# Kernel optimization log

Hardware: AMD Instinct MI355X
Metric: run time of the kernel (lower is better)

The kernel has to match this reference:

```python
import jax, jax.numpy as jnp
import numpy as np

N_NODES = 50000
N_EDGES = 600000
NFEAT = 256
NHID = 128
NCLASS = 40


def setup_inputs() -> dict:
    key = jax.random.key(0)
    ks = jax.random.split(key, 10)
    x = jax.random.normal(ks[0], (N_NODES, NFEAT), dtype=jnp.float32)
    edge_src = jax.random.randint(ks[1], (N_EDGES,), 0, N_NODES, dtype=jnp.int32)
    edge_dst = jax.random.randint(ks[2], (N_EDGES,), 0, N_NODES, dtype=jnp.int32)
    # normalized adjacency weights (positive, ~1/deg scale)
    edge_weight = jax.random.uniform(ks[3], (N_EDGES,), dtype=jnp.float32) * 0.2
    # GraphConvolution params (Glorot-ish init)
    W1 = jax.random.normal(ks[4], (NFEAT, NHID), dtype=jnp.float32) / np.float32(np.sqrt(NFEAT))
    b1 = jnp.zeros((NHID,), dtype=jnp.float32)
    W2 = jax.random.normal(ks[5], (NHID, NHID), dtype=jnp.float32) / np.float32(np.sqrt(NHID))
    b2 = jnp.zeros((NHID,), dtype=jnp.float32)
    W3 = jax.random.normal(ks[6], (NHID, NCLASS), dtype=jnp.float32) / np.float32(np.sqrt(NHID))
    b3 = jnp.zeros((NCLASS,), dtype=jnp.float32)
    return {"x": x, "edge_weight": edge_weight, "W1": W1, "b1": b1,
            "W2": W2, "b2": b2, "W3": W3, "b3": b3,
            "edge_src": edge_src, "edge_dst": edge_dst}


def _gcn_layer(h, W, b, edge_src, edge_dst, edge_weight):
    # support = h @ W ; out = spmm(adj, support) + b
    support = h @ W                                   # [N, out]
    msgs = support[edge_src] * edge_weight[:, None]   # [E, out]
    agg = jax.ops.segment_sum(msgs, edge_dst, num_segments=N_NODES)
    return agg + b


def reference(x, edge_weight, W1, b1, W2, b2, W3, b3, edge_src, edge_dst):
    # eval mode: F.dropout(training=False) is identity
    h = jax.nn.relu(_gcn_layer(x, W1, b1, edge_src, edge_dst, edge_weight))
    h = jax.nn.relu(_gcn_layer(h, W2, b2, edge_src, edge_dst, edge_weight))
    h = _gcn_layer(h, W3, b3, edge_src, edge_dst, edge_weight)
    return jax.nn.log_softmax(h, axis=1)
```

## Files before the change

### kernel.cpp

```cpp
#include <hip/hip_runtime.h>
#include <hip/hip_bf16.h>
#include <math.h>

#define N_NODES 50000
#define N_EDGES 600000
#define NFEAT   256
#define NHID    128
#define NCLASS  40
#define E_PAD_MAX (N_EDGES + 7 * N_NODES)
#define GEMM_BLOCKS  ((N_NODES + 63) / 64)
#define NBUCK 196
#define EPB_A 2048
#define BUCK_CAP 4096

typedef __attribute__((ext_vector_type(8))) short bf16x8;
typedef __attribute__((ext_vector_type(4))) float f32x4;
typedef __attribute__((ext_vector_type(2))) float f32x2;

__device__ inline ushort f2bf(float f) {
    uint u = __float_as_uint(f);
    uint r = (u + 0x7fffu + ((u >> 16) & 1u)) >> 16;
    return (ushort)r;
}

__global__ __launch_bounds__(256) void scatter_binA(const int* __restrict__ src,
                                                    const int* __restrict__ dst,
                                                    const float* __restrict__ w,
                                                    int* __restrict__ bucket_cnt,
                                                    int2* __restrict__ staging, int E) {
    __shared__ int lh[NBUCK];
    int tid = threadIdx.x;
    for (int b = tid; b < NBUCK; b += 256) lh[b] = 0;
    __syncthreads();
    int base = blockIdx.x * EPB_A;
    int d[8];
    #pragma unroll
    for (int j = 0; j < 8; ++j) {
        int i = base + j * 256 + tid;
        d[j] = (i < E) ? dst[i] : -1;
        if (d[j] >= 0) atomicAdd(&lh[d[j] >> 8], 1);
    }
    __syncthreads();
    for (int b = tid; b < NBUCK; b += 256) {
        int c = lh[b];
        lh[b] = c ? (b * BUCK_CAP + atomicAdd(&bucket_cnt[b], c)) : 0;
    }
    __syncthreads();
    #pragma unroll
    for (int j = 0; j < 8; ++j) {
        int i = base + j * 256 + tid;
        if (d[j] >= 0) {
            int slot = atomicAdd(&lh[d[j] >> 8], 1);
            uint rec = ((uint)f2bf(w[i]) << 16) | (uint)src[i];
            staging[slot] = make_int2((int)rec, d[j] & 255);
        }
    }
}

__global__ __launch_bounds__(256) void bucket_hist_cvtw(const int* __restrict__ bucket_cnt,
                                                        const int2* __restrict__ staging,
                                                        int* __restrict__ bsum, int nb,
                                                        const float* __restrict__ W1,
                                                        const float* __restrict__ W2,
                                                        const float* __restrict__ W3,
                                                        ushort* __restrict__ BT1,
                                                        ushort* __restrict__ BT2,
                                                        ushort* __restrict__ BT3) {
    if ((int)blockIdx.x >= nb) {
        int idx = ((int)blockIdx.x - nb) * 256 + threadIdx.x;
        if (idx < 32768) {
            int nr = idx >> 8, k = idx & 255;
            BT1[idx] = f2bf(W1[(size_t)k * 128 + nr]);
        } else if (idx < 49152) {
            int t = idx - 32768;
            int nr = t >> 7, k = t & 127;
            BT2[t] = f2bf(W2[(size_t)k * 128 + nr]);
        } else if (idx < 57344) {
            int t = idx - 49152;
            int nr = t >> 7, k = t & 127;
            BT3[t] = (nr < 40) ? f2bf(W3[(size_t)k * 40 + nr]) : (ushort)0;
        }
        return;
    }
    __shared__ int hist[256];
    __shared__ int red[4];
    int tid = threadIdx.x;
    hist[tid] = 0;
    __syncthreads();
    int b = blockIdx.x;
    int c = bucket_cnt[b];
    const int2* st = staging + (size_t)b * BUCK_CAP;
    for (int p = tid; p < c; p += 256) atomicAdd(&hist[st[p].y], 1);
    __syncthreads();
    int v = (hist[tid] + 7) & ~7;
    #pragma unroll
    for (int off = 32; off; off >>= 1) v += __shfl_down(v, off, 64);
    int wv = tid >> 6, lane = tid & 63;
    if (lane == 0) red[wv] = v;
    __syncthreads();
    if (tid == 0) bsum[b] = red[0] + red[1] + red[2] + red[3];
}

__global__ __launch_bounds__(256) void scan_scatter(const int* __restrict__ bsum,
                                                    const int* __restrict__ bucket_cnt,
                                                    const int2* __restrict__ staging,
                                                    int* __restrict__ rsp,
                                                    uint* __restrict__ edges, int n) {
    __shared__ int hist[256];
    __shared__ int buf[256];
    __shared__ int lcur[256];
    __shared__ int boff_s;
    int tid = threadIdx.x;
    hist[tid] = 0;
    if (tid < 64) {
        int s = 0;
        for (int i = tid; i < (int)blockIdx.x; i += 64) s += bsum[i];
        #pragma unroll
        for (int off = 32; off; off >>= 1) s += __shfl_down(s, off, 64);
        if (tid == 0) boff_s = s;
    }
    __syncthreads();
    int b = blockIdx.x;
    int c = bucket_cnt[b];
    const int2* st = staging + (size_t)b * BUCK_CAP;
    for (int p = tid; p < c; p += 256) atomicAdd(&hist[st[p].y], 1);
    __syncthreads();
    int v = (hist[tid] + 7) & ~7;
    buf[tid] = v;
    __syncthreads();
    #pragma unroll
    for (int off = 1; off < 256; off <<= 1) {
        int t = (tid >= off) ? buf[tid - off] : 0;
        __syncthreads();
        buf[tid] += t;
        __syncthreads();
    }
    int ex = buf[tid] - v + boff_s;
    int i = b * 256 + tid;
    if (i < n) rsp[i] = ex;
    if (i == n - 1) rsp[n] = ex + v;
    lcur[tid] = ex;
    __syncthreads();
    int s0 = boff_s, e0 = buf[255] + boff_s;
    for (int p = s0 + tid; p < e0; p += 256) edges[p] = 0;
    __syncthreads();
    for (int p = tid; p < c; p += 256) {
        int2 r = st[p];
        int slot = atomicAdd(&lcur[r.y], 1);
        edges[slot] = (uint)r.x;
    }
}

template<int NT, bool OUTBF, bool AF32>
__device__ __forceinline__ void gemm_body(const void* __restrict__ Ain,
                                          const ushort* __restrict__ BT,
                                          int M, int K, int Nout,
                                          void* __restrict__ Cout, int row0) {
    __shared__ ushort a_s[64 * 40];
    __shared__ ushort b_s[64 * NT * 40];
    int tid = threadIdx.x;
    int wave = tid >> 6, lane = tid & 63;
    int lr = lane & 15, lk = (lane >> 4) * 8;
    f32x4 acc[4][NT];
    #pragma unroll
    for (int mt = 0; mt < 4; ++mt)
        #pragma unroll
        for (int nt = 0; nt < NT; ++nt) acc[mt][nt] = (f32x4){0.f, 0.f, 0.f, 0.f};

    for (int k0 = 0; k0 < K; k0 += 32) {
        {
            int r = tid >> 2, c8 = (tid & 3) * 8;
            int gr = row0 + r; if (gr >= M) gr = M - 1;
            if (AF32) {
                const float* Af = (const float*)Ain;
                float4 v0 = *(const float4*)(Af + (size_t)gr * K + k0 + c8);
                float4 v1 = *(const float4*)(Af + (size_t)gr * K + k0 + c8 + 4);
                ushort4 o0, o1;
                o0.x = f2bf(v0.x); o0.y = f2bf(v0.y); o0.z = f2bf(v0.z); o0.w = f2bf(v0.w);
                o1.x = f2bf(v1.x); o1.y = f2bf(v1.y); o1.z = f2bf(v1.z); o1.w = f2bf(v1.w);
                *(ushort4*)(a_s + r * 40 + c8) = o0;
                *(ushort4*)(a_s + r * 40 + c8 + 4) = o1;
            } else {
                const ushort* Ab = (const ushort*)Ain;
                float4 v = *(const float4*)(Ab + (size_t)gr * K + k0 + c8);
                *(float4*)(a_s + r * 40 + c8) = v;
            }
        }
        #pragma unroll
        for (int i = 0; i < NT; ++i) {
            int idx = tid * NT + i;
            int r = idx >> 2, c8 = (idx & 3) * 8;
            float4 v = *(const float4*)(BT + (size_t)r * K + k0 + c8);
            *(float4*)(b_s + r * 40 + c8) = v;
        }
        __syncthreads();
        bf16x8 bfr[NT];
        #pragma unroll
        for (int nt = 0; nt < NT; ++nt)
            bfr[nt] = *(const bf16x8*)(b_s + ((wave * NT + nt) * 16 + lr) * 40 + lk);
        #pragma unroll
        for (int mt = 0; mt < 4; ++mt) {
            bf16x8 afr = *(const bf16x8*)(a_s + (mt * 16 + lr) * 40 + lk);
            #pragma unroll
            for (int nt = 0; nt < NT; ++nt)
                acc[mt][nt] = __builtin_amdgcn_mfma_f32_16x16x32_bf16(
                    afr, bfr[nt], acc[mt][nt], 0, 0, 0);
        }
        __syncthreads();
    }
    int col0 = wave * NT * 16;
    #pragma unroll
    for (int mt = 0; mt < 4; ++mt) {
        int gr0 = row0 + mt * 16 + (lane >> 4) * 4;
        #pragma unroll
        for (int nt = 0; nt < NT; ++nt) {
            int gc = col0 + nt * 16 + lr;
            #pragma unroll
            for (int i = 0; i < 4; ++i) {
                int gr = gr0 + i;
                if (gr < M && gc < Nout) {
                    if (OUTBF)
                        ((ushort*)Cout)[(size_t)gr * Nout + gc] = f2bf(acc[mt][nt][i]);
                    else
                        ((float*)Cout)[(size_t)gr * Nout + gc] = acc[mt][nt][i];
                }
            }
        }
    }
}

template<int NT, bool OUTBF, bool AF32>
__global__ __launch_bounds__(256) void gemm_mfma(const void* __restrict__ Ain,
                                                 const ushort* __restrict__ BT,
                                                 int M, int K, int Nout,
                                                 void* __restrict__ Cout) {
    gemm_body<NT, OUTBF, AF32>(Ain, BT, M, K, Nout, Cout, blockIdx.x * 64);
}

__global__ __launch_bounds__(256) void spmm128b(const uint* __restrict__ sup,
                                                const int* __restrict__ rsp,
                                                const uint* __restrict__ edges,
                                                const float* __restrict__ bias,
                                                uint* __restrict__ outb, int n) {
    int wid = blockIdx.x * 4 + (threadIdx.x >> 6);
    int lane = threadIdx.x & 63;
    if (wid >= n) return;
    int k = rsp[wid], e = rsp[wid + 1];
    f32x2 acc = (f32x2){0.f, 0.f};
    if (k < e) {
        const uint4* q4 = (const uint4*)(edges + k);
        uint4 qa = q4[0], qb = q4[1];
        for (; k < e; k += 8) {
            int kn = k + 8;
            int kc = (kn < e) ? kn : k;
            const uint4* n4 = (const uint4*)(edges + kc);
            uint4 na = n4[0], nb = n4[1];
            uint q[8] = {qa.x, qa.y, qa.z, qa.w, qb.x, qb.y, qb.z, qb.w};
            uint p[8];
            #pragma unroll
            for (int j = 0; j < 8; ++j)
                p[j] = sup[(size_t)(q[j] & 0xffffu) * 64 + lane];
            #pragma unroll
            for (int j = 0; j < 8; ++j) {
                float w = __uint_as_float(q[j] & 0xffff0000u);
                f32x2 v;
                v.x = __uint_as_float(p[j] << 16);
                v.y = __uint_as_float(p[j] & 0xffff0000u);
                acc += v * (f32x2){w, w};
            }
            qa = na; qb = nb;
        }
    }
    float ax = fmaxf(acc.x + bias[lane * 2], 0.f);
    float ay = fmaxf(acc.y + bias[lane * 2 + 1], 0.f);
    outb[(size_t)wid * 64 + lane] = ((uint)f2bf(ay) << 16) | (uint)f2bf(ax);
}

__global__ __launch_bounds__(256) void spmm40_lsm(const ushort* __restrict__ sup,
                                                  const int* __restrict__ rsp,
                                                  const uint* __restrict__ edges,
                                                  const float* __restrict__ bias,
                                                  float* __restrict__ out, int n) {
    int wid = blockIdx.x * 4 + (threadIdx.x >> 6);
    int lane = threadIdx.x & 63;
    if (wid >= n) return;
    int k = rsp[wid], e = rsp[wid + 1];
    float acc = 0.f;
    int lf = (lane < 40) ? lane : 39;
    if (k < e) {
        const uint4* q4 = (const uint4*)(edges + k);
        uint4 qa = q4[0], qb = q4[1];
        for (; k < e; k += 8) {
            int kn = k + 8;
            int kc = (kn < e) ? kn : k;
            const uint4* n4 = (const uint4*)(edges + kc);
            uint4 na = n4[0], nb = n4[1];
            uint q[8] = {qa.x, qa.y, qa.z, qa.w, qb.x, qb.y, qb.z, qb.w};
            float p[8];
            #pragma unroll
            for (int j = 0; j < 8; ++j) {
                uint us = sup[(size_t)(q[j] & 0xffffu) * 40 + lf];
                p[j] = __uint_as_float(us << 16);
            }
            #pragma unroll
            for (int j = 0; j < 8; ++j)
                acc += p[j] * __uint_as_float(q[j] & 0xffff0000u);
            qa = na; qb = nb;
        }
    }
    float v = (lane < 40) ? acc + bias[lane] : -INFINITY;
    float m = v;
    #pragma unroll
    for (int off = 32; off; off >>= 1) m = fmaxf(m, __shfl_xor(m, off, 64));
    float ex = (lane < 40) ? expf(v - m) : 0.f;
    float s = ex;
    #pragma unroll
    for (int off = 32; off; off >>= 1) s += __shfl_xor(s, off, 64);
    float ls = logf(s);
    if (lane < 40) out[(size_t)wid * 40 + lane] = v - m - ls;
}

extern "C" void kernel_launch(void* const* d_in, const int* in_sizes, int n_in,
                              void* d_out, int out_size, void* d_ws, size_t ws_size,
                              hipStream_t stream) {
    const float* x   = (const float*)d_in[0];
    const float* ew  = (const float*)d_in[1];
    const float* W1  = (const float*)d_in[2];
    const float* b1  = (const float*)d_in[3];
    const float* W2  = (const float*)d_in[4];
    const float* b2  = (const float*)d_in[5];
    const float* W3  = (const float*)d_in[6];
    const float* b3  = (const float*)d_in[7];
    const int* esrc  = (const int*)d_in[8];
    const int* edst  = (const int*)d_in[9];
    float* out = (float*)d_out;

    char* ws = (char*)d_ws;
    size_t off = 0;
    auto alloc = [&](size_t bytes) {
        size_t cur = off;
        off += (bytes + 255) & ~(size_t)255;
        return cur;
    };
    int* bucket_cnt = (int*)(ws + alloc(256 * sizeof(int)));
    int* bsum    = (int*)(ws + alloc(256 * sizeof(int)));
    int* rsp     = (int*)(ws + alloc((N_NODES + 1) * sizeof(int)));
    uint* edges  = (uint*)(ws + alloc((size_t)E_PAD_MAX * sizeof(uint)));
    int2* staging = (int2*)(ws + alloc((size_t)NBUCK * BUCK_CAP * sizeof(int2)));
    ushort* BT1  = (ushort*)(ws + alloc(128 * 256 * 2));
    ushort* BT2  = (ushort*)(ws + alloc(128 * 128 * 2));
    ushort* BT3  = (ushort*)(ws + alloc(64 * 128 * 2));
    char* Sreg   = ws + alloc((size_t)N_NODES * 128 * 2);
    char* Hreg   = ws + alloc((size_t)N_NODES * 128 * 2);
    char* Treg   = ws + alloc((size_t)N_NODES * 128 * 2);

    ushort* supA = (ushort*)Sreg;
    ushort* hA   = (ushort*)Hreg;
    ushort* supB = (ushort*)Treg;
    ushort* hB   = (ushort*)Sreg;
    ushort* sup3 = (ushort*)Treg;

    int cvtw_blocks = (57344 + 255) / 256;

    hipMemsetAsync(bucket_cnt, 0, 256 * sizeof(int), stream);
    scatter_binA<<<(N_EDGES + EPB_A - 1) / EPB_A, 256, 0, stream>>>(
        esrc, edst, ew, bucket_cnt, staging, N_EDGES);
    bucket_hist_cvtw<<<NBUCK + cvtw_blocks, 256, 0, stream>>>(
        bucket_cnt, staging, bsum, NBUCK, W1, W2, W3, BT1, BT2, BT3);
    scan_scatter<<<NBUCK, 256, 0, stream>>>(bsum, bucket_cnt, staging, rsp,
                                            edges, N_NODES);

    int spmm_blocks = (N_NODES + 3) / 4;

    gemm_mfma<2, true, true><<<GEMM_BLOCKS, 256, 0, stream>>>(x, BT1, N_NODES, 256,
                                                              128, supA);
    spmm128b<<<spmm_blocks, 256, 0, stream>>>((const uint*)supA, rsp, edges, b1,
                                              (uint*)hA, N_NODES);
    gemm_mfma<2, true, false><<<GEMM_BLOCKS, 256, 0, stream>>>(hA, BT2, N_NODES, 128,
                                                               128, supB);
    spmm128b<<<spmm_blocks, 256, 0, stream>>>((const uint*)supB, rsp, edges, b2,
                                              (uint*)hB, N_NODES);
    gemm_mfma<1, true, false><<<GEMM_BLOCKS, 256, 0, stream>>>(hB, BT3, N_NODES, 128,
                                                               40, sup3);
    spmm40_lsm<<<spmm_blocks, 256, 0, stream>>>(sup3, rsp, edges, b3, out, N_NODES);
}
```

Measured before the change: 233.2 us.

## Fuse all stages into one cooperative persistent kernel with grid syncs

Replaces the nine separate launches (binning, histogram, scan-scatter, three GEMMs, three SpMMs) with one cooperative kernel. A persistent grid walks virtual blocks and uses grid.sync between phases. The separate bucket-histogram pass is dropped by giving each bucket a fixed window in the edge array (BUCK_WIN), so no global prefix sum is needed. Row pointers become int2 start/end pairs. Weight conversion is overlapped with binning, and the scan is overlapped with the first GEMM. The aim is to remove launch overhead and serial gaps between kernels. The risks are grid-sync cost, lower occupancy from the union shared memory, and a fixed window that overflows if a bucket gets more padded edges than BUCK_WIN.

New measurement: 698.7 us. +199.6%, slower.

```diff
diff --git a/kernel.cpp b/kernel.cpp
--- a/kernel.cpp
+++ b/kernel.cpp
@@ -1,17 +1,22 @@
 #include <hip/hip_runtime.h>
-#include <hip/hip_bf16.h>
+#include <hip/hip_cooperative_groups.h>
 #include <math.h>
+
+namespace cg = cooperative_groups;
 
 #define N_NODES 50000
 #define N_EDGES 600000
 #define NFEAT   256
 #define NHID    128
 #define NCLASS  40
-#define E_PAD_MAX (N_EDGES + 7 * N_NODES)
-#define GEMM_BLOCKS  ((N_NODES + 63) / 64)
 #define NBUCK 196
 #define EPB_A 2048
 #define BUCK_CAP 4096
+#define BUCK_WIN 5888
+#define BINA_VB ((N_EDGES + EPB_A - 1) / EPB_A)
+#define CVTW_VB 224
+#define GEMM_VB ((N_NODES + 63) / 64)
+#define SPMM_VB ((N_NODES + 3) / 4)
 
 typedef __attribute__((ext_vector_type(8))) short bf16x8;
 typedef __attribute__((ext_vector_type(4))) float f32x4;
@@ -23,27 +28,42 @@
     return (ushort)r;
 }
 
-__global__ __launch_bounds__(256) void scatter_binA(const int* __restrict__ src,
-                                                    const int* __restrict__ dst,
-                                                    const float* __restrict__ w,
-                                                    int* __restrict__ bucket_cnt,
-                                                    int2* __restrict__ staging, int E) {
-    __shared__ int lh[NBUCK];
+struct Params {
+    const int* esrc; const int* edst; const float* ew;
+    const float* W1; const float* b1;
+    const float* W2; const float* b2;
+    const float* W3; const float* b3;
+    const float* x; float* out;
+    int* bucket_cnt; int2* rsp2; uint* edges; int2* staging;
+    ushort* BT1; ushort* BT2; ushort* BT3;
+    ushort* supA; ushort* hA; ushort* supB; ushort* hB; ushort* sup3;
+};
+
+struct SMem {
+    union {
+        int lh[NBUCK];
+        struct { int hist[256]; int buf[256]; int lcur[256]; } sc;
+        struct { ushort a_s[64 * 40]; ushort b_s[128 * 40]; } ge;
+    } u;
+};
+
+__device__ __forceinline__ void binA_body(const Params& P, int vb, SMem& sm) {
     int tid = threadIdx.x;
+    int* lh = sm.u.lh;
     for (int b = tid; b < NBUCK; b += 256) lh[b] = 0;
     __syncthreads();
-    int base = blockIdx.x * EPB_A;
+    int base = vb * EPB_A;
     int d[8];
     #pragma unroll
     for (int j = 0; j < 8; ++j) {
         int i = base + j * 256 + tid;
-        d[j] = (i < E) ? dst[i] : -1;
+        d[j] = (i < N_EDGES) ? P.edst[i] : -1;
         if (d[j] >= 0) atomicAdd(&lh[d[j] >> 8], 1);
     }
     __syncthreads();
     for (int b = tid; b < NBUCK; b += 256) {
         int c = lh[b];
-        lh[b] = c ? (b * BUCK_CAP + atomicAdd(&bucket_cnt[b], c)) : 0;
+        lh[b] = c ? (b * BUCK_CAP + atomicAdd(&P.bucket_cnt[b], c)) : 0;
     }
     __syncthreads();
     #pragma unroll
@@ -51,78 +71,38 @@
         int i = base + j * 256 + tid;
         if (d[j] >= 0) {
             int slot = atomicAdd(&lh[d[j] >> 8], 1);
-            uint rec = ((uint)f2bf(w[i]) << 16) | (uint)src[i];
-            staging[slot] = make_int2((int)rec, d[j] & 255);
-        }
-    }
-}
-
-__global__ __launch_bounds__(256) void bucket_hist_cvtw(const int* __restrict__ bucket_cnt,
-                                                        const int2* __restrict__ staging,
-                                                        int* __restrict__ bsum, int nb,
-                                                        const float* __restrict__ W1,
-                                                        const float* __restrict__ W2,
-                                                        const float* __restrict__ W3,
-                                                        ushort* __restrict__ BT1,
-                                                        ushort* __restrict__ BT2,
-                                                        ushort* __restrict__ BT3) {
-    if ((int)blockIdx.x >= nb) {
-        int idx = ((int)blockIdx.x - nb) * 256 + threadIdx.x;
-        if (idx < 32768) {
-            int nr = idx >> 8, k = idx & 255;
-            BT1[idx] = f2bf(W1[(size_t)k * 128 + nr]);
-        } else if (idx < 49152) {
-            int t = idx - 32768;
-            int nr = t >> 7, k = t & 127;
-            BT2[t] = f2bf(W2[(size_t)k * 128 + nr]);
-        } else if (idx < 57344) {
-            int t = idx - 49152;
-            int nr = t >> 7, k = t & 127;
-            BT3[t] = (nr < 40) ? f2bf(W3[(size_t)k * 40 + nr]) : (ushort)0;
-        }
-        return;
-    }
-    __shared__ int hist[256];
-    __shared__ int red[4];
+            uint rec = ((uint)f2bf(P.ew[i]) << 16) | (uint)P.esrc[i];
+            P.staging[slot] = make_int2((int)rec, d[j] & 255);
+        }
+    }
+    __syncthreads();
+}
+
+__device__ __forceinline__ void cvtw_body(const Params& P, int vb) {
+    int idx = vb * 256 + (int)threadIdx.x;
+    if (idx < 32768) {
+        int nr = idx >> 8, k = idx & 255;
+        P.BT1[idx] = f2bf(P.W1[(size_t)k * 128 + nr]);
+    } else if (idx < 49152) {
+        int t = idx - 32768;
+        int nr = t >> 7, k = t & 127;
+        P.BT2[t] = f2bf(P.W2[(size_t)k * 128 + nr]);
+    } else if (idx < 57344) {
+        int t = idx - 49152;
+        int nr = t >> 7, k = t & 127;
+        P.BT3[t] = (nr < 40) ? f2bf(P.W3[(size_t)k * 40 + nr]) : (ushort)0;
+    }
+}
+
+__device__ __forceinline__ void scan_body(const Params& P, int b, SMem& sm) {
     int tid = threadIdx.x;
+    int* hist = sm.u.sc.hist;
+    int* buf  = sm.u.sc.buf;
+    int* lcur = sm.u.sc.lcur;
     hist[tid] = 0;
     __syncthreads();
-    int b = blockIdx.x;
-    int c = bucket_cnt[b];
-    const int2* st = staging + (size_t)b * BUCK_CAP;
-    for (int p = tid; p < c; p += 256) atomicAdd(&hist[st[p].y], 1);
-    __syncthreads();
-    int v = (hist[tid] + 7) & ~7;
-    #pragma unroll
-    for (int off = 32; off; off >>= 1) v += __shfl_down(v, off, 64);
-    int wv = tid >> 6, lane = tid & 63;
-    if (lane == 0) red[wv] = v;
-    __syncthreads();
-    if (tid == 0) bsum[b] = red[0] + red[1] + red[2] + red[3];
-}
-
-__global__ __launch_bounds__(256) void scan_scatter(const int* __restrict__ bsum,
-                                                    const int* __restrict__ bucket_cnt,
-                                                    const int2* __restrict__ staging,
-                                                    int* __restrict__ rsp,
-                                                    uint* __restrict__ edges, int n) {
-    __shared__ int hist[256];
-    __shared__ int buf[256];
-    __shared__ int lcur[256];
-    __shared__ int boff_s;
-    int tid = threadIdx.x;
-    hist[tid] = 0;
-    if (tid < 64) {
-        int s = 0;
-        for (int i = tid; i < (int)blockIdx.x; i += 64) s += bsum[i];
-        #pragma unroll
-        for (int off = 32; off; off >>= 1) s += __shfl_down(s, off, 64);
-        if (tid == 0) boff_s = s;
-    }
-    __syncthreads();
-    int b = blockIdx.x;
-    int c = bucket_cnt[b];
-    const int2* st = staging + (size_t)b * BUCK_CAP;
+    int c = P.bucket_cnt[b];
+    const int2* st = P.staging + (size_t)b * BUCK_CAP;
     for (int p = tid; p < c; p += 256) atomicAdd(&hist[st[p].y], 1);
     __syncthreads();
     int v = (hist[tid] + 7) & ~7;
@@ -135,29 +115,29 @@
         buf[tid] += t;
         __syncthreads();
     }
-    int ex = buf[tid] - v + boff_s;
+    int bb = b * BUCK_WIN;
+    int ex = buf[tid] - v + bb;
     int i = b * 256 + tid;
-    if (i < n) rsp[i] = ex;
-    if (i == n - 1) rsp[n] = ex + v;
+    if (i < N_NODES) P.rsp2[i] = make_int2(ex, ex + v);
     lcur[tid] = ex;
     __syncthreads();
-    int s0 = boff_s, e0 = buf[255] + boff_s;
-    for (int p = s0 + tid; p < e0; p += 256) edges[p] = 0;
+    int e0 = bb + buf[255];
+    for (int p = bb + tid; p < e0; p += 256) P.edges[p] = 0;
     __syncthreads();
     for (int p = tid; p < c; p += 256) {
         int2 r = st[p];
         int slot = atomicAdd(&lcur[r.y], 1);
-        edges[slot] = (uint)r.x;
-    }
+        P.edges[slot] = (uint)r.x;
+    }
+    __syncthreads();
 }
 
 template<int NT, bool OUTBF, bool AF32>
 __device__ __forceinline__ void gemm_body(const void* __restrict__ Ain,
                                           const ushort* __restrict__ BT,
                                           int M, int K, int Nout,
-                                          void* __restrict__ Cout, int row0) {
-    __shared__ ushort a_s[64 * 40];
-    __shared__ ushort b_s[64 * NT * 40];
+                                          void* __restrict__ Cout, int row0,
+                                          ushort* a_s, ushort* b_s) {
     int tid = threadIdx.x;
     int wave = tid >> 6, lane = tid & 63;
     int lr = lane & 15, lk = (lane >> 4) * 8;
@@ -229,31 +209,21 @@
     }
 }
 
-template<int NT, bool OUTBF, bool AF32>
-__global__ __launch_bounds__(256) void gemm_mfma(const void* __restrict__ Ain,
-                                                 const ushort* __restrict__ BT,
-                                                 int M, int K, int Nout,
-                                                 void* __restrict__ Cout) {
-    gemm_body<NT, OUTBF, AF32>(Ain, BT, M, K, Nout, Cout, blockIdx.x * 64);
-}
-
-__global__ __launch_bounds__(256) void spmm128b(const uint* __restrict__ sup,
-                                                const int* __restrict__ rsp,
-                                                const uint* __restrict__ edges,
-                                                const float* __restrict__ bias,
-                                                uint* __restrict__ outb, int n) {
-    int wid = blockIdx.x * 4 + (threadIdx.x >> 6);
-    int lane = threadIdx.x & 63;
-    if (wid >= n) return;
-    int k = rsp[wid], e = rsp[wid + 1];
+__device__ __forceinline__ void spmm128_body(const Params& P,
+                                             const uint* __restrict__ sup,
+                                             const float* __restrict__ bias,
+                                             uint* __restrict__ outb,
+                                             int wid, int lane) {
+    int2 ke = P.rsp2[wid];
+    int k = ke.x, e = ke.y;
     f32x2 acc = (f32x2){0.f, 0.f};
     if (k < e) {
-        const uint4* q4 = (const uint4*)(edges + k);
+        const uint4* q4 = (const uint4*)(P.edges + k);
         uint4 qa = q4[0], qb = q4[1];
         for (; k < e; k += 8) {
             int kn = k + 8;
             int kc = (kn < e) ? kn : k;
-            const uint4* n4 = (const uint4*)(edges + kc);
+            const uint4* n4 = (const uint4*)(P.edges + kc);
             uint4 na = n4[0], nb = n4[1];
             uint q[8] = {qa.x, qa.y, qa.z, qa.w, qb.x, qb.y, qb.z, qb.w};
             uint p[8];
@@ -276,25 +246,20 @@
     outb[(size_t)wid * 64 + lane] = ((uint)f2bf(ay) << 16) | (uint)f2bf(ax);
 }
 
-__global__ __launch_bounds__(256) void spmm40_lsm(const ushort* __restrict__ sup,
-                                                  const int* __restrict__ rsp,
-                                                  const uint* __restrict__ edges,
-                                                  const float* __restrict__ bias,
-                                                  float* __restrict__ out, int n) {
-    int wid = blockIdx.x * 4 + (threadIdx.x >> 6);
-    int lane = threadIdx.x & 63;
-    if (wid >= n) return;
-    int k = rsp[wid], e = rsp[wid + 1];
+__device__ __forceinline__ void spmm40_body(const Params& P, int wid, int lane) {
+    int2 ke = P.rsp2[wid];
+    int k = ke.x, e = ke.y;
     float acc = 0.f;
     int lf = (lane < 40) ? lane : 39;
+    const ushort* sup = P.sup3;
     if (k < e) {
-        const uint4* q4 = (const uint4*)(edges + k);
+        const uint4* q4 = (const uint4*)(P.edges + k);
         uint4 qa = q4[0], qb = q4[1];
         for (; k < e; k += 8) {
             int kn = k + 8;
             int kc = (kn < e) ? kn : k;
-            const uint4* n4 = (const uint4*)(edges + kc);
-            uint4 na = n4[0], nb = n4[1];
+            const uint4* n4 = (const uint4*)(P.edges + kc);
+            uint4 na = n4[0], nb4 = n4[1];
             uint q[8] = {qa.x, qa.y, qa.z, qa.w, qb.x, qb.y, qb.z, qb.w};
             float p[8];
             #pragma unroll
@@ -305,10 +270,10 @@
             #pragma unroll
             for (int j = 0; j < 8; ++j)
                 acc += p[j] * __uint_as_float(q[j] & 0xffff0000u);
-            qa = na; qb = nb;
-        }
-    }
-    float v = (lane < 40) ? acc + bias[lane] : -INFINITY;
+            qa = na; qb = nb4;
+        }
+    }
+    float v = (lane < 40) ? acc + P.b3[lane] : -INFINITY;
     float m = v;
     #pragma unroll
     for (int off = 32; off; off >>= 1) m = fmaxf(m, __shfl_xor(m, off, 64));
@@ -317,24 +282,61 @@
     #pragma unroll
     for (int off = 32; off; off >>= 1) s += __shfl_xor(s, off, 64);
     float ls = logf(s);
-    if (lane < 40) out[(size_t)wid * 40 + lane] = v - m - ls;
+    if (lane < 40) P.out[(size_t)wid * 40 + lane] = v - m - ls;
+}
+
+__global__ __launch_bounds__(256) void mega(Params P) {
+    __shared__ SMem sm;
+    cg::grid_group grid = cg::this_grid();
+    int tid = threadIdx.x;
+    int nb = gridDim.x;
+
+    for (int vb = blockIdx.x; vb < BINA_VB + CVTW_VB; vb += nb) {
+        if (vb < BINA_VB) binA_body(P, vb, sm);
+        else cvtw_body(P, vb - BINA_VB);
+    }
+    grid.sync();
+
+    for (int vb = blockIdx.x; vb < NBUCK + GEMM_VB; vb += nb) {
+        if (vb < NBUCK) scan_body(P, vb, sm);
+        else gemm_body<2, true, true>(P.x, P.BT1, N_NODES, 256, 128, P.supA,
+                                      (vb - NBUCK) * 64, sm.u.ge.a_s, sm.u.ge.b_s);
+    }
+    grid.sync();
+
+    for (int vb = blockIdx.x; vb < SPMM_VB; vb += nb) {
+        int wid = vb * 4 + (tid >> 6);
+        if (wid < N_NODES)
+            spmm128_body(P, (const uint*)P.supA, P.b1, (uint*)P.hA, wid, tid & 63);
+    }
+    grid.sync();
+
+    for (int vb = blockIdx.x; vb < GEMM_VB; vb += nb)
+        gemm_body<2, true, false>(P.hA, P.BT2, N_NODES, 128, 128, P.supB,
+                                  vb * 64, sm.u.ge.a_s, sm.u.ge.b_s);
+    grid.sync();
+
+    for (int vb = blockIdx.x; vb < SPMM_VB; vb += nb) {
+        int wid = vb * 4 + (tid >> 6);
+        if (wid < N_NODES)
+            spmm128_body(P, (const uint*)P.supB, P.b2, (uint*)P.hB, wid, tid & 63);
+    }
+    grid.sync();
+
+    for (int vb = blockIdx.x; vb < GEMM_VB; vb += nb)
+        gemm_body<1, true, false>(P.hB, P.BT3, N_NODES, 128, 40, P.sup3,
+                                  vb * 64, sm.u.ge.a_s, sm.u.ge.b_s);
+    grid.sync();
+
+    for (int vb = blockIdx.x; vb < SPMM_VB; vb += nb) {
+        int wid = vb * 4 + (tid >> 6);
+        if (wid < N_NODES) spmm40_body(P, wid, tid & 63);
+    }
 }
 
 extern "C" void kernel_launch(void* const* d_in, const int* in_sizes, int n_in,
                               void* d_out, int out_size, void* d_ws, size_t ws_size,
                               hipStream_t stream) {
-    const float* x   = (const float*)d_in[0];
-    const float* ew  = (const float*)d_in[1];
-    const float* W1  = (const float*)d_in[2];
-    const float* b1  = (const float*)d_in[3];
-    const float* W2  = (const float*)d_in[4];
-    const float* b2  = (const float*)d_in[5];
-    const float* W3  = (const float*)d_in[6];
-    const float* b3  = (const float*)d_in[7];
-    const int* esrc  = (const int*)d_in[8];
-    const int* edst  = (const int*)d_in[9];
-    float* out = (float*)d_out;
-
     char* ws = (char*)d_ws;
     size_t off = 0;
     auto alloc = [&](size_t bytes) {
@@ -343,9 +345,8 @@
         return cur;
     };
     int* bucket_cnt = (int*)(ws + alloc(256 * sizeof(int)));
-    int* bsum    = (int*)(ws + alloc(256 * sizeof(int)));
-    int* rsp     = (int*)(ws + alloc((N_NODES + 1) * sizeof(int)));
-    uint* edges  = (uint*)(ws + alloc((size_t)E_PAD_MAX * sizeof(uint)));
+    int2* rsp2   = (int2*)(ws + alloc((size_t)N_NODES * sizeof(int2)));
+    uint* edges  = (uint*)(ws + alloc((size_t)NBUCK * BUCK_WIN * sizeof(uint)));
     int2* staging = (int2*)(ws + alloc((size_t)NBUCK * BUCK_CAP * sizeof(int2)));
     ushort* BT1  = (ushort*)(ws + alloc(128 * 256 * 2));
     ushort* BT2  = (ushort*)(ws + alloc(128 * 128 * 2));
@@ -354,33 +355,40 @@
     char* Hreg   = ws + alloc((size_t)N_NODES * 128 * 2);
     char* Treg   = ws + alloc((size_t)N_NODES * 128 * 2);
 
-    ushort* supA = (ushort*)Sreg;
-    ushort* hA   = (ushort*)Hreg;
-    ushort* supB = (ushort*)Treg;
-    ushort* hB   = (ushort*)Sreg;
-    ushort* sup3 = (ushort*)Treg;
-
-    int cvtw_blocks = (57344 + 255) / 256;
+    Params P;
+    P.x   = (const float*)d_in[0];
+    P.ew  = (const float*)d_in[1];
+    P.W1  = (const float*)d_in[2];
+    P.b1  = (const float*)d_in[3];
+    P.W2  = (const float*)d_in[4];
+    P.b2  = (const float*)d_in[5];
+    P.W3  = (const float*)d_in[6];
+    P.b3  = (const float*)d_in[7];
+    P.esrc = (const int*)d_in[8];
+    P.edst = (const int*)d_in[9];
+    P.out = (float*)d_out;
+    P.bucket_cnt = bucket_cnt;
+    P.rsp2 = rsp2;
+    P.edges = edges;
+    P.staging = staging;
+    P.BT1 = BT1; P.BT2 = BT2; P.BT3 = BT3;
+    P.supA = (ushort*)Sreg;
+    P.hA   = (ushort*)Hreg;
+    P.supB = (ushort*)Treg;
+    P.hB   = (ushort*)Sreg;
+    P.sup3 = (ushort*)Treg;
+
+    static int s_nblk = 0;
+    if (s_nblk == 0) {
+        int maxb = 0;
+        hipError_t err = hipOccupancyMaxActiveBlocksPerMultiprocessor(&maxb, mega,
+                                                                      256, (size_t)0);
+        if (err != hipSuccess || maxb < 1) maxb = 2;
+        if (maxb > 8) maxb = 8;
+        s_nblk = maxb * 256;
+    }
 
     hipMemsetAsync(bucket_cnt, 0, 256 * sizeof(int), stream);
-    scatter_binA<<<(N_EDGES + EPB_A - 1) / EPB_A, 256, 0, stream>>>(
-        esrc, edst, ew, bucket_cnt, staging, N_EDGES);
-    bucket_hist_cvtw<<<NBUCK + cvtw_blocks, 256, 0, stream>>>(
-        bucket_cnt, staging, bsum, NBUCK, W1, W2, W3, BT1, BT2, BT3);
-    scan_scatter<<<NBUCK, 256, 0, stream>>>(bsum, bucket_cnt, staging, rsp,
-                                            edges, N_NODES);
-
-    int spmm_blocks = (N_NODES + 3) / 4;
-
-    gemm_mfma<2, true, true><<<GEMM_BLOCKS, 256, 0, stream>>>(x, BT1, N_NODES, 256,
-                                                              128, supA);
-    spmm128b<<<spmm_blocks, 256, 0, stream>>>((const uint*)supA, rsp, edges, b1,
-                                              (uint*)hA, N_NODES);
-    gemm_mfma<2, true, false><<<GEMM_BLOCKS, 256, 0, stream>>>(hA, BT2, N_NODES, 128,
-                                                               128, supB);
-    spmm128b<<<spmm_blocks, 256, 0, stream>>>((const uint*)supB, rsp, edges, b2,
-                                              (uint*)hB, N_NODES);
-    gemm_mfma<1, true, false><<<GEMM_BLOCKS, 256, 0, stream>>>(hB, BT3, N_NODES, 128,
-                                                               40, sup3);
-    spmm40_lsm<<<spmm_blocks, 256, 0, stream>>>(sup3, rsp, edges, b3, out, N_NODES);
-}
+    void* kargs[] = { &P };
+    hipLaunchCooperativeKernel(mega, dim3(s_nblk), dim3(256), kargs, 0, stream);
+}
```

## Fuse SpMM with following GEMM and merge CSR build stages via fixed bucket windows

Applied to the files above, without the earlier changes.

Replaces the global prefix-sum CSR build with fixed per-bucket edge windows (BUCK_WIN) and [start,end) pairs, which removes the bucket_hist pass and lets the scan run in the same launch as the first GEMM. Weight conversion is folded into the binning kernel. Each SpMM for layers 1 and 2 is fused with the next layer's GEMM: a block aggregates 64 rows into LDS, then multiplies them by the transposed weights with MFMA. This cuts the kernel count from eight to five and avoids writing and re-reading the intermediate hidden activations. The cost is lower gather parallelism, since 64 rows go per block in a sequential per-wave loop, and a fixed window size that assumes each bucket's padded edge count fits.

New measurement: 231.2 us. Within noise of the previous version (-0.9%).

```diff
diff --git a/kernel.cpp b/kernel.cpp
--- a/kernel.cpp
+++ b/kernel.cpp
@@ -1,5 +1,4 @@
 #include <hip/hip_runtime.h>
-#include <hip/hip_bf16.h>
 #include <math.h>
 
 #define N_NODES 50000
@@ -7,11 +6,13 @@
 #define NFEAT   256
 #define NHID    128
 #define NCLASS  40
-#define E_PAD_MAX (N_EDGES + 7 * N_NODES)
-#define GEMM_BLOCKS  ((N_NODES + 63) / 64)
 #define NBUCK 196
 #define EPB_A 2048
 #define BUCK_CAP 4096
+#define BUCK_WIN 5888
+#define BINA_BLOCKS ((N_EDGES + EPB_A - 1) / EPB_A)
+#define CVTW_BLOCKS 224
+#define GEMM_BLOCKS ((N_NODES + 63) / 64)
 
 typedef __attribute__((ext_vector_type(8))) short bf16x8;
 typedef __attribute__((ext_vector_type(4))) float f32x4;
@@ -23,51 +24,20 @@
     return (ushort)r;
 }
 
-__global__ __launch_bounds__(256) void scatter_binA(const int* __restrict__ src,
-                                                    const int* __restrict__ dst,
-                                                    const float* __restrict__ w,
-                                                    int* __restrict__ bucket_cnt,
-                                                    int2* __restrict__ staging, int E) {
-    __shared__ int lh[NBUCK];
+__global__ __launch_bounds__(256) void binA_cvtw(const int* __restrict__ src,
+                                                 const int* __restrict__ dst,
+                                                 const float* __restrict__ w,
+                                                 int* __restrict__ bucket_cnt,
+                                                 int2* __restrict__ staging, int E,
+                                                 const float* __restrict__ W1,
+                                                 const float* __restrict__ W2,
+                                                 const float* __restrict__ W3,
+                                                 ushort* __restrict__ BT1,
+                                                 ushort* __restrict__ BT2,
+                                                 ushort* __restrict__ BT3) {
     int tid = threadIdx.x;
-    for (int b = tid; b < NBUCK; b += 256) lh[b] = 0;
-    __syncthreads();
-    int base = blockIdx.x * EPB_A;
-    int d[8];
-    #pragma unroll
-    for (int j = 0; j < 8; ++j) {
-        int i = base + j * 256 + tid;
-        d[j] = (i < E) ? dst[i] : -1;
-        if (d[j] >= 0) atomicAdd(&lh[d[j] >> 8], 1);
-    }
-    __syncthreads();
-    for (int b = tid; b < NBUCK; b += 256) {
-        int c = lh[b];
-        lh[b] = c ? (b * BUCK_CAP + atomicAdd(&bucket_cnt[b], c)) : 0;
-    }
-    __syncthreads();
-    #pragma unroll
-    for (int j = 0; j < 8; ++j) {
-        int i = base + j * 256 + tid;
-        if (d[j] >= 0) {
-            int slot = atomicAdd(&lh[d[j] >> 8], 1);
-            uint rec = ((uint)f2bf(w[i]) << 16) | (uint)src[i];
-            staging[slot] = make_int2((int)rec, d[j] & 255);
-        }
-    }
-}
-
-__global__ __launch_bounds__(256) void bucket_hist_cvtw(const int* __restrict__ bucket_cnt,
-                                                        const int2* __restrict__ staging,
-                                                        int* __restrict__ bsum, int nb,
-                                                        const float* __restrict__ W1,
-                                                        const float* __restrict__ W2,
-                                                        const float* __restrict__ W3,
-                                                        ushort* __restrict__ BT1,
-                                                        ushort* __restrict__ BT2,
-                                                        ushort* __restrict__ BT3) {
-    if ((int)blockIdx.x >= nb) {
-        int idx = ((int)blockIdx.x - nb) * 256 + threadIdx.x;
+    if ((int)blockIdx.x >= BINA_BLOCKS) {
+        int idx = ((int)blockIdx.x - BINA_BLOCKS) * 256 + tid;
         if (idx < 32768) {
             int nr = idx >> 8, k = idx & 255;
             BT1[idx] = f2bf(W1[(size_t)k * 128 + nr]);
@@ -82,80 +52,39 @@
         }
         return;
     }
-    __shared__ int hist[256];
-    __shared__ int red[4];
-    int tid = threadIdx.x;
-    hist[tid] = 0;
-    __syncthreads();
-    int b = blockIdx.x;
-    int c = bucket_cnt[b];
-    const int2* st = staging + (size_t)b * BUCK_CAP;
-    for (int p = tid; p < c; p += 256) atomicAdd(&hist[st[p].y], 1);
-    __syncthreads();
-    int v = (hist[tid] + 7) & ~7;
-    #pragma unroll
-    for (int off = 32; off; off >>= 1) v += __shfl_down(v, off, 64);
-    int wv = tid >> 6, lane = tid & 63;
-    if (lane == 0) red[wv] = v;
-    __syncthreads();
-    if (tid == 0) bsum[b] = red[0] + red[1] + red[2] + red[3];
-}
-
-__global__ __launch_bounds__(256) void scan_scatter(const int* __restrict__ bsum,
-                                                    const int* __restrict__ bucket_cnt,
-                                                    const int2* __restrict__ staging,
-                                                    int* __restrict__ rsp,
-                                                    uint* __restrict__ edges, int n) {
-    __shared__ int hist[256];
-    __shared__ int buf[256];
-    __shared__ int lcur[256];
-    __shared__ int boff_s;
-    int tid = threadIdx.x;
-    hist[tid] = 0;
-    if (tid < 64) {
-        int s = 0;
-        for (int i = tid; i < (int)blockIdx.x; i += 64) s += bsum[i];
-        #pragma unroll
-        for (int off = 32; off; off >>= 1) s += __shfl_down(s, off, 64);
-        if (tid == 0) boff_s = s;
-    }
-    __syncthreads();
-    int b = blockIdx.x;
-    int c = bucket_cnt[b];
-    const int2* st = staging + (size_t)b * BUCK_CAP;
-    for (int p = tid; p < c; p += 256) atomicAdd(&hist[st[p].y], 1);
-    __syncthreads();
-    int v = (hist[tid] + 7) & ~7;
-    buf[tid] = v;
-    __syncthreads();
-    #pragma unroll
-    for (int off = 1; off < 256; off <<= 1) {
-        int t = (tid >= off) ? buf[tid - off] : 0;
-        __syncthreads();
-        buf[tid] += t;
-        __syncthreads();
-    }
-    int ex = buf[tid] - v + boff_s;
-    int i = b * 256 + tid;
-    if (i < n) rsp[i] = ex;
-    if (i == n - 1) rsp[n] = ex + v;
-    lcur[tid] = ex;
-    __syncthreads();
-    int s0 = boff_s, e0 = buf[255] + boff_s;
-    for (int p = s0 + tid; p < e0; p += 256) edges[p] = 0;
-    __syncthreads();
-    for (int p = tid; p < c; p += 256) {
-        int2 r = st[p];
-        int slot = atomicAdd(&lcur[r.y], 1);
-        edges[slot] = (uint)r.x;
-    }
-}
-
-template<int NT, bool OUTBF, bool AF32>
+    __shared__ int lh[NBUCK];
+    for (int b = tid; b < NBUCK; b += 256) lh[b] = 0;
+    __syncthreads();
+    int base = blockIdx.x * EPB_A;
+    int d[8];
+    #pragma unroll
+    for (int j = 0; j < 8; ++j) {
+        int i = base + j * 256 + tid;
+        d[j] = (i < E) ? dst[i] : -1;
+        if (d[j] >= 0) atomicAdd(&lh[d[j] >> 8], 1);
+    }
+    __syncthreads();
+    for (int b = tid; b < NBUCK; b += 256) {
+        int c = lh[b];
+        lh[b] = c ? (b * BUCK_CAP + atomicAdd(&bucket_cnt[b], c)) : 0;
+    }
+    __syncthreads();
+    #pragma unroll
+    for (int j = 0; j < 8; ++j) {
+        int i = base + j * 256 + tid;
+        if (d[j] >= 0) {
+            int slot = atomicAdd(&lh[d[j] >> 8], 1);
+            uint rec = ((uint)f2bf(w[i]) << 16) | (uint)src[i];
+            staging[slot] = make_int2((int)rec, d[j] & 255);
+        }
+    }
+}
+
+template<int NT, bool AF32>
 __device__ __forceinline__ void gemm_body(const void* __restrict__ Ain,
                                           const ushort* __restrict__ BT,
                                           int M, int K, int Nout,
-                                          void* __restrict__ Cout, int row0) {
+                                          ushort* __restrict__ Cout, int row0) {
     __shared__ ushort a_s[64 * 40];
     __shared__ ushort b_s[64 * NT * 40];
     int tid = threadIdx.x;
@@ -218,73 +147,162 @@
             #pragma unroll
             for (int i = 0; i < 4; ++i) {
                 int gr = gr0 + i;
-                if (gr < M && gc < Nout) {
-                    if (OUTBF)
-                        ((ushort*)Cout)[(size_t)gr * Nout + gc] = f2bf(acc[mt][nt][i]);
-                    else
-                        ((float*)Cout)[(size_t)gr * Nout + gc] = acc[mt][nt][i];
+                if (gr < M && gc < Nout)
+                    Cout[(size_t)gr * Nout + gc] = f2bf(acc[mt][nt][i]);
+            }
+        }
+    }
+}
+
+__global__ __launch_bounds__(256) void scan_gemm1(const int* __restrict__ bucket_cnt,
+                                                  const int2* __restrict__ staging,
+                                                  int2* __restrict__ rsp2,
+                                                  uint* __restrict__ edges,
+                                                  const float* __restrict__ x,
+                                                  const ushort* __restrict__ BT1,
+                                                  ushort* __restrict__ supA) {
+    if ((int)blockIdx.x >= NBUCK) {
+        gemm_body<2, true>(x, BT1, N_NODES, 256, 128, supA,
+                           ((int)blockIdx.x - NBUCK) * 64);
+        return;
+    }
+    __shared__ int hist[256];
+    __shared__ int buf[256];
+    __shared__ int lcur[256];
+    int tid = threadIdx.x;
+    hist[tid] = 0;
+    __syncthreads();
+    int b = blockIdx.x;
+    int c = bucket_cnt[b];
+    const int2* st = staging + (size_t)b * BUCK_CAP;
+    for (int p = tid; p < c; p += 256) atomicAdd(&hist[st[p].y], 1);
+    __syncthreads();
+    int v = (hist[tid] + 7) & ~7;
+    buf[tid] = v;
+    __syncthreads();
+    #pragma unroll
+    for (int off = 1; off < 256; off <<= 1) {
+        int t = (tid >= off) ? buf[tid - off] : 0;
+        __syncthreads();
+        buf[tid] += t;
+        __syncthreads();
+    }
+    int bb = b * BUCK_WIN;
+    int ex = buf[tid] - v + bb;
+    int i = b * 256 + tid;
+    if (i < N_NODES) rsp2[i] = make_int2(ex, ex + v);
+    lcur[tid] = ex;
+    __syncthreads();
+    int e0 = bb + buf[255];
+    for (int p = bb + tid; p < e0; p += 256) edges[p] = 0;
+    __syncthreads();
+    for (int p = tid; p < c; p += 256) {
+        int2 r = st[p];
+        int slot = atomicAdd(&lcur[r.y], 1);
+        edges[slot] = (uint)r.x;
+    }
+}
+
+template<int NT>
+__global__ __launch_bounds__(256) void fused_spmm_gemm(const uint* __restrict__ sup,
+                                                       const int2* __restrict__ rsp2,
+                                                       const uint* __restrict__ edges,
+                                                       const float* __restrict__ bias,
+                                                       const ushort* __restrict__ BT,
+                                                       int Nout,
+                                                       ushort* __restrict__ Cout) {
+    __shared__ ushort a4_s[4][64 * 40];
+    int tid = threadIdx.x;
+    int wave = tid >> 6, lane = tid & 63;
+    int row0 = blockIdx.x * 64;
+    float bx = bias[2 * lane], by = bias[2 * lane + 1];
+    int ks = lane >> 4;
+    int kk = 2 * (lane & 15);
+    for (int i = 0; i < 16; ++i) {
+        int node = row0 + wave * 16 + i;
+        int nd = (node < N_NODES) ? node : (N_NODES - 1);
+        int2 ke = rsp2[nd];
+        int k = ke.x, e = ke.y;
+        f32x2 acc2 = (f32x2){0.f, 0.f};
+        if (k < e) {
+            const uint4* q4 = (const uint4*)(edges + k);
+            uint4 qa = q4[0], qb = q4[1];
+            for (; k < e; k += 8) {
+                int kn = k + 8;
+                int kc = (kn < e) ? kn : k;
+                const uint4* n4 = (const uint4*)(edges + kc);
+                uint4 na = n4[0], nb = n4[1];
+                uint q[8] = {qa.x, qa.y, qa.z, qa.w, qb.x, qb.y, qb.z, qb.w};
+                uint p[8];
+                #pragma unroll
+                for (int j = 0; j < 8; ++j)
+                    p[j] = sup[(size_t)(q[j] & 0xffffu) * 64 + lane];
+                #pragma unroll
+                for (int j = 0; j < 8; ++j) {
+                    float w = __uint_as_float(q[j] & 0xffff0000u);
+                    f32x2 v;
+                    v.x = __uint_as_float(p[j] << 16);
+                    v.y = __uint_as_float(p[j] & 0xffff0000u);
+                    acc2 += v * (f32x2){w, w};
                 }
-            }
-        }
-    }
-}
-
-template<int NT, bool OUTBF, bool AF32>
-__global__ __launch_bounds__(256) void gemm_mfma(const void* __restrict__ Ain,
-                                                 const ushort* __restrict__ BT,
-                                                 int M, int K, int Nout,
-                                                 void* __restrict__ Cout) {
-    gemm_body<NT, OUTBF, AF32>(Ain, BT, M, K, Nout, Cout, blockIdx.x * 64);
-}
-
-__global__ __launch_bounds__(256) void spmm128b(const uint* __restrict__ sup,
-                                                const int* __restrict__ rsp,
-                                                const uint* __restrict__ edges,
-                                                const float* __restrict__ bias,
-                                                uint* __restrict__ outb, int n) {
-    int wid = blockIdx.x * 4 + (threadIdx.x >> 6);
-    int lane = threadIdx.x & 63;
-    if (wid >= n) return;
-    int k = rsp[wid], e = rsp[wid + 1];
-    f32x2 acc = (f32x2){0.f, 0.f};
-    if (k < e) {
-        const uint4* q4 = (const uint4*)(edges + k);
-        uint4 qa = q4[0], qb = q4[1];
-        for (; k < e; k += 8) {
-            int kn = k + 8;
-            int kc = (kn < e) ? kn : k;
-            const uint4* n4 = (const uint4*)(edges + kc);
-            uint4 na = n4[0], nb = n4[1];
-            uint q[8] = {qa.x, qa.y, qa.z, qa.w, qb.x, qb.y, qb.z, qb.w};
-            uint p[8];
-            #pragma unroll
-            for (int j = 0; j < 8; ++j)
-                p[j] = sup[(size_t)(q[j] & 0xffffu) * 64 + lane];
-            #pragma unroll
-            for (int j = 0; j < 8; ++j) {
-                float w = __uint_as_float(q[j] & 0xffff0000u);
-                f32x2 v;
-                v.x = __uint_as_float(p[j] << 16);
-                v.y = __uint_as_float(p[j] & 0xffff0000u);
-                acc += v * (f32x2){w, w};
-            }
-            qa = na; qb = nb;
-        }
-    }
-    float ax = fmaxf(acc.x + bias[lane * 2], 0.f);
-    float ay = fmaxf(acc.y + bias[lane * 2 + 1], 0.f);
-    outb[(size_t)wid * 64 + lane] = ((uint)f2bf(ay) << 16) | (uint)f2bf(ax);
+                qa = na; qb = nb;
+            }
+        }
+        uint pk = ((uint)f2bf(fmaxf(acc2.y + by, 0.f)) << 16)
+                |  (uint)f2bf(fmaxf(acc2.x + bx, 0.f));
+        *(uint*)(&a4_s[ks][(wave * 16 + i) * 40 + kk]) = pk;
+    }
+    __syncthreads();
+    int lr = lane & 15, lk = (lane >> 4) * 8;
+    f32x4 acc[4][NT];
+    #pragma unroll
+    for (int mt = 0; mt < 4; ++mt)
+        #pragma unroll
+        for (int nt = 0; nt < NT; ++nt) acc[mt][nt] = (f32x4){0.f, 0.f, 0.f, 0.f};
+    #pragma unroll
+    for (int ksi = 0; ksi < 4; ++ksi) {
+        int k0 = ksi * 32;
+        bf16x8 bfr[NT];
+        #pragma unroll
+        for (int nt = 0; nt < NT; ++nt)
+            bfr[nt] = *(const bf16x8*)(BT +
+                (size_t)((wave * NT + nt) * 16 + lr) * 128 + k0 + lk);
+        #pragma unroll
+        for (int mt = 0; mt < 4; ++mt) {
+            bf16x8 afr = *(const bf16x8*)(&a4_s[ksi][(mt * 16 + lr) * 40 + lk]);
+            #pragma unroll
+            for (int nt = 0; nt < NT; ++nt)
+                acc[mt][nt] = __builtin_amdgcn_mfma_f32_16x16x32_bf16(
+                    afr, bfr[nt], acc[mt][nt], 0, 0, 0);
+        }
+    }
+    int col0 = wave * NT * 16;
+    #pragma unroll
+    for (int mt = 0; mt < 4; ++mt) {
+        int gr0 = row0 + mt * 16 + (lane >> 4) * 4;
+        #pragma unroll
+        for (int nt = 0; nt < NT; ++nt) {
+            int gc = col0 + nt * 16 + lr;
+            #pragma unroll
+            for (int i = 0; i < 4; ++i) {
+                int gr = gr0 + i;
+                if (gr < N_NODES && gc < Nout)
+                    Cout[(size_t)gr * Nout + gc] = f2bf(acc[mt][nt][i]);
+            }
+        }
+    }
 }
 
 __global__ __launch_bounds__(256) void spmm40_lsm(const ushort* __restrict__ sup,
-                                                  const int* __restrict__ rsp,
+                                                  const int2* __restrict__ rsp2,
                                                   const uint* __restrict__ edges,
                                                   const float* __restrict__ bias,
                                                   float* __restrict__ out, int n) {
     int wid = blockIdx.x * 4 + (threadIdx.x >> 6);
     int lane = threadIdx.x & 63;
     if (wid >= n) return;
-    int k = rsp[wid], e = rsp[wid + 1];
+    int2 ke = rsp2[wid];
+    int k = ke.x, e = ke.y;
     float acc = 0.f;
     int lf = (lane < 40) ? lane : 39;
     if (k < e) {
@@ -294,7 +312,7 @@
             int kn = k + 8;
             int kc = (kn < e) ? kn : k;
             const uint4* n4 = (const uint4*)(edges + kc);
-            uint4 na = n4[0], nb = n4[1];
+            uint4 na = n4[0], nb4 = n4[1];
             uint q[8] = {qa.x, qa.y, qa.z, qa.w, qb.x, qb.y, qb.z, qb.w};
             float p[8];
             #pragma unroll
@@ -305,7 +323,7 @@
             #pragma unroll
             for (int j = 0; j < 8; ++j)
                 acc += p[j] * __uint_as_float(q[j] & 0xffff0000u);
-            qa = na; qb = nb;
+            qa = na; qb = nb4;
         }
     }
     float v = (lane < 40) ? acc + bias[lane] : -INFINITY;
@@ -343,44 +361,28 @@
         return cur;
     };
     int* bucket_cnt = (int*)(ws + alloc(256 * sizeof(int)));
-    int* bsum    = (int*)(ws + alloc(256 * sizeof(int)));
-    int* rsp     = (int*)(ws + alloc((N_NODES + 1) * sizeof(int)));
-    uint* edges  = (uint*)(ws + alloc((size_t)E_PAD_MAX * sizeof(uint)));
+    int2* rsp2   = (int2*)(ws + alloc((size_t)N_NODES * sizeof(int2)));
+    uint* edges  = (uint*)(ws + alloc((size_t)NBUCK * BUCK_WIN * sizeof(uint)));
     int2* staging = (int2*)(ws + alloc((size_t)NBUCK * BUCK_CAP * sizeof(int2)));
     ushort* BT1  = (ushort*)(ws + alloc(128 * 256 * 2));
     ushort* BT2  = (ushort*)(ws + alloc(128 * 128 * 2));
     ushort* BT3  = (ushort*)(ws + alloc(64 * 128 * 2));
     char* Sreg   = ws + alloc((size_t)N_NODES * 128 * 2);
     char* Hreg   = ws + alloc((size_t)N_NODES * 128 * 2);
-    char* Treg   = ws + alloc((size_t)N_NODES * 128 * 2);
 
     ushort* supA = (ushort*)Sreg;
-    ushort* hA   = (ushort*)Hreg;
-    ushort* supB = (ushort*)Treg;
-    ushort* hB   = (ushort*)Sreg;
-    ushort* sup3 = (ushort*)Treg;
-
-    int cvtw_blocks = (57344 + 255) / 256;
+    ushort* supB = (ushort*)Hreg;
+    ushort* sup3 = (ushort*)Sreg;
 
     hipMemsetAsync(bucket_cnt, 0, 256 * sizeof(int), stream);
-    scatter_binA<<<(N_EDGES + EPB_A - 1) / EPB_A, 256, 0, stream>>>(
-        esrc, edst, ew, bucket_cnt, staging, N_EDGES);
-    bucket_hist_cvtw<<<NBUCK + cvtw_blocks, 256, 0, stream>>>(
-        bucket_cnt, staging, bsum, NBUCK, W1, W2, W3, BT1, BT2, BT3);
-    scan_scatter<<<NBUCK, 256, 0, stream>>>(bsum, bucket_cnt, staging, rsp,
-                                            edges, N_NODES);
-
-    int spmm_blocks = (N_NODES + 3) / 4;
-
-    gemm_mfma<2, true, true><<<GEMM_BLOCKS, 256, 0, stream>>>(x, BT1, N_NODES, 256,
-                                                              128, supA);
-    spmm128b<<<spmm_blocks, 256, 0, stream>>>((const uint*)supA, rsp, edges, b1,
-                                              (uint*)hA, N_NODES);
-    gemm_mfma<2, true, false><<<GEMM_BLOCKS, 256, 0, stream>>>(hA, BT2, N_NODES, 128,
-                                                               128, supB);
-    spmm128b<<<spmm_blocks, 256, 0, stream>>>((const uint*)supB, rsp, edges, b2,
-                                              (uint*)hB, N_NODES);
-    gemm_mfma<1, true, false><<<GEMM_BLOCKS, 256, 0, stream>>>(hB, BT3, N_NODES, 128,
-                                                               40, sup3);
-    spmm40_lsm<<<spmm_blocks, 256, 0, stream>>>(sup3, rsp, edges, b3, out, N_NODES);
-}
+    binA_cvtw<<<BINA_BLOCKS + CVTW_BLOCKS, 256, 0, stream>>>(
+        esrc, edst, ew, bucket_cnt, staging, N_EDGES, W1, W2, W3, BT1, BT2, BT3);
+    scan_gemm1<<<NBUCK + GEMM_BLOCKS, 256, 0, stream>>>(
+        bucket_cnt, staging, rsp2, edges, x, BT1, supA);
+    fused_spmm_gemm<2><<<GEMM_BLOCKS, 256, 0, stream>>>(
+        (const uint*)supA, rsp2, edges, b1, BT2, 128, supB);
+    fused_spmm_gemm<1><<<GEMM_BLOCKS, 256, 0, stream>>>(
+        (const uint*)supB, rsp2, edges, b2, BT3, 40, sup3);
+    spmm40_lsm<<<(N_NODES + 3) / 4, 256, 0, stream>>>(sup3, rsp2, edges, b3,
+                                                      out, N_NODES);
+}
```
